# Kernel tuning notes

Hardware: AMD Instinct MI355X
Metric: run time of the kernel (lower is better)

Reference implementation:

```python
import jax, jax.numpy as jnp
import numpy as np

N = 50000      # nodes
E = 800000     # edges (avg degree 16)
DIN = 512      # input_dim
DH = 256       # hidden_dim
KMAX = 50      # max_clusters; K = max(5, min(50, ceil(N/50))) = 50 for N=50000


def _gcn_propagate(h, src, dst, n):
    """Symmetric-normalized GCN aggregation with self-loops (PyG GCNConv).
    h: already linearly transformed node features (n, d)."""
    loop = jnp.arange(n)
    s = jnp.concatenate([src, loop])
    d = jnp.concatenate([dst, loop])
    deg = jax.ops.segment_sum(jnp.ones_like(d, dtype=h.dtype), d, num_segments=n)
    dinv = jnp.where(deg > 0, deg ** -0.5, 0.0)
    norm = dinv[s] * dinv[d]                      # (E+N,)
    return jax.ops.segment_sum(norm[:, None] * h[s], d, num_segments=n)


def setup_inputs() -> dict:
    key = jax.random.key(0)
    ks = jax.random.split(key, 6)
    x = jax.random.normal(ks[0], (N, DIN), dtype=jnp.float32)
    edge_index = jax.random.randint(ks[1], (2, E), 0, N, dtype=jnp.int64)
    positions = jax.random.uniform(ks[2], (N, 2), dtype=jnp.float32)
    # GCNConv params (glorot-ish weights, zero bias as in PyG init)
    W1 = jax.random.normal(ks[3], (DIN, DH), dtype=jnp.float32) * np.float32(1.0 / np.sqrt(DIN))
    b1 = jnp.zeros((DH,), dtype=jnp.float32)
    W2 = jax.random.normal(ks[4], (DH, KMAX), dtype=jnp.float32) * np.float32(1.0 / np.sqrt(DH))
    b2 = jnp.zeros((KMAX,), dtype=jnp.float32)
    spatial_weight = jnp.asarray(1.0, dtype=jnp.float32)
    return {"x": x, "positions": positions, "W1": W1, "b1": b1,
            "W2": W2, "b2": b2, "spatial_weight": spatial_weight,
            "edge_index": edge_index}


def reference(x, positions, W1, b1, W2, b2, spatial_weight, edge_index):
    src, dst = edge_index[0], edge_index[1]
    n = x.shape[0]
    # layer 1: GCNConv(input_dim -> hidden_dim) + ReLU
    h = jax.nn.relu(_gcn_propagate(x @ W1, src, dst, n) + b1)
    # layer 2: GCNConv(hidden_dim -> max_clusters)
    s = _gcn_propagate(h @ W2, src, dst, n) + b2
    # K = max(5, min(50, ceil(N/50))) = 50 here -> s[:, :K] is identity slice
    S = jax.nn.softmax(s[:, :KMAX], axis=1)       # (N, K), Eq. 7
    # spatial loss (Eq. 9): softmax > 0 always, so the >0 guards are no-ops
    d2 = jnp.sum((positions[src] - positions[dst]) ** 2, axis=1)   # (E,) squared dist
    dot = jnp.sum(S[src] * S[dst], axis=1)                          # (E,) sum_k S_ik S_jk
    L_spatial = spatial_weight * jnp.sum(d2 * dot) / src.shape[0]
    return S, L_spatial
```

## Files before the change

### kernel.cpp

```cpp
#include <hip/hip_runtime.h>
#include <math.h>


typedef __attribute__((ext_vector_type(8))) short bf16x8;
typedef __attribute__((ext_vector_type(4))) float f32x4;
typedef __attribute__((ext_vector_type(4))) unsigned int u32x4;
typedef _Float16 f16;
typedef __attribute__((ext_vector_type(2))) _Float16 f16x2;
typedef __attribute__((ext_vector_type(4))) _Float16 f16x4;
typedef __attribute__((ext_vector_type(8))) _Float16 f16x8;

__device__ inline unsigned short f32_to_bf16(float f) {
    unsigned u = __float_as_uint(f);
    unsigned r = u + 0x7FFFu + ((u >> 16) & 1u);
    return (unsigned short)(r >> 16);
}
__device__ inline float bf16_to_f32(unsigned short h) {
    return __uint_as_float((unsigned)h << 16);
}

__device__ inline void glds16(const void* g, void* l) {
    __builtin_amdgcn_global_load_lds(
        (const __attribute__((address_space(1))) unsigned int*)g,
        (__attribute__((address_space(3))) unsigned int*)l, 16, 0, 0);
}

__global__ void detect_i64_kernel(const unsigned* __restrict__ w, int* __restrict__ flag) {
    __shared__ int red[256];
    int cnt = 0;
    for (int i = threadIdx.x; i < 4096; i += 256)
        cnt += (w[2 * i + 1] == 0u) ? 1 : 0;
    red[threadIdx.x] = cnt;
    __syncthreads();
    for (int s = 128; s > 0; s >>= 1) {
        if ((int)threadIdx.x < s) red[threadIdx.x] += red[threadIdx.x + s];
        __syncthreads();
    }
    if (threadIdx.x == 0) *flag = (red[0] > 2048) ? 1 : 0;
}

__global__ void convert_edges_kernel(const void* __restrict__ ei, int* __restrict__ es,
                                     int* __restrict__ ed, int* __restrict__ cnt,
                                     int E, const int* __restrict__ flag) {
    int idx = blockIdx.x * blockDim.x + threadIdx.x;
    if (idx >= 2 * E) return;
    int v;
    if (*flag) v = (int)((const long long*)ei)[idx];
    else       v = ((const int*)ei)[idx];
    if (idx < E) es[idx] = v;
    else { ed[idx - E] = v; atomicAdd(&cnt[v], 1); }
}

__global__ __launch_bounds__(1024) void scan_block_kernel(const int* __restrict__ cnt,
        int* __restrict__ row_ptr, int* __restrict__ btot, int n) {
    __shared__ int buf[1024];
    int i = blockIdx.x * 1024 + threadIdx.x;
    buf[threadIdx.x] = (i < n) ? cnt[i] : 0;
    __syncthreads();
    for (int off = 1; off < 1024; off <<= 1) {
        int t = ((int)threadIdx.x >= off) ? buf[threadIdx.x - off] : 0;
        __syncthreads();
        buf[threadIdx.x] += t;
        __syncthreads();
    }
    if (i < n) row_ptr[i + 1] = buf[threadIdx.x];
    if (threadIdx.x == 1023) btot[blockIdx.x] = buf[1023];
}

__global__ __launch_bounds__(1024) void scan_tops_kernel(int* __restrict__ btot, int nb) {
    __shared__ int buf[1024];
    buf[threadIdx.x] = ((int)threadIdx.x < nb) ? btot[threadIdx.x] : 0;
    __syncthreads();
    for (int off = 1; off < 1024; off <<= 1) {
        int t = ((int)threadIdx.x >= off) ? buf[threadIdx.x - off] : 0;
        __syncthreads();
        buf[threadIdx.x] += t;
        __syncthreads();
    }
    if ((int)threadIdx.x < nb) btot[threadIdx.x] = buf[threadIdx.x];
}

__global__ void scan_finalize_kernel(int* __restrict__ row_ptr, const int* __restrict__ btot,
        const int* __restrict__ cnt, int* __restrict__ cursor, float* __restrict__ dinv, int n) {
    int i = blockIdx.x * blockDim.x + threadIdx.x;
    if (i >= n) return;
    int blk = i >> 10;
    int off = blk ? btot[blk - 1] : 0;
    int incl = row_ptr[i + 1] + off;
    row_ptr[i + 1] = incl;
    cursor[i] = incl - cnt[i];
    dinv[i] = rsqrtf((float)(cnt[i] + 1));
    if (i == 0) row_ptr[0] = 0;
}

__global__ void scatter_kernel(const int* __restrict__ es, const int* __restrict__ ed,
                               const float* __restrict__ dinv, int* __restrict__ cursor,
                               int* __restrict__ csr_src, float* __restrict__ csr_nrm, int E) {
    int e = blockIdx.x * blockDim.x + threadIdx.x;
    if (e < E) {
        int s = es[e];
        int d = ed[e];
        int p = atomicAdd(&cursor[d], 1);
        csr_src[p] = s;
        csr_nrm[p] = dinv[s];
    }
}

__global__ void wsplit_kernel(const float* __restrict__ W,
                              unsigned short* __restrict__ Th,
                              unsigned short* __restrict__ Tl, int K, int N, int nk) {
    int idx = blockIdx.x * 256 + threadIdx.x;
    if (idx >= K * N) return;
    int k = idx / N, n = idx % N;
    float f = W[idx];
    unsigned short h = f32_to_bf16(f);
    unsigned short l = f32_to_bf16(f - bf16_to_f32(h));
    int p = n >> 7, np = n & 127, t = k >> 5, kg = (k & 31) >> 3, ke = k & 7;
    size_t o = ((size_t)((p * nk + t) * 4 + kg) << 10) + np * 8 + ke;
    Th[o] = h;
    Tl[o] = l;
}

__global__ void wsplit2_kernel(const float* __restrict__ W2,
                               f16* __restrict__ W2t_hi, f16* __restrict__ W2t_lo,
                               int K, int NC) {
    int idx = blockIdx.x * 256 + threadIdx.x;
    if (idx >= 64 * K) return;
    int n = idx / K, k = idx % K;
    float v = (n < NC) ? W2[(size_t)k * NC + n] : 0.f;
    f16 h = (f16)v;
    W2t_hi[idx] = h;
    W2t_lo[idx] = (f16)(v - (float)h);
}

#define G1_BM 128
#define G1_BN 128
#define G1_BK 32

__global__ __launch_bounds__(256) void gemm1_mfma(
        const float* __restrict__ X, const unsigned short* __restrict__ WtH,
        const unsigned short* __restrict__ WtL, f16* __restrict__ C,
        int M, int K, int N) {
    __shared__ __align__(16) unsigned char lds[32768];

    const int tid  = threadIdx.x;
    const int lane = tid & 63;
    const int wave = tid >> 6;
    const int wm   = wave & 1;
    const int wn   = wave >> 1;
    const int m0   = blockIdx.x * G1_BM;
    const int pn   = blockIdx.y;
    const int nk   = K / G1_BK;

    const float* Xbase[4];
    #pragma unroll
    for (int i = 0; i < 4; ++i) {
        int c   = i * 256 + tid;
        int row = c >> 3;
        int sl  = (c & 7) ^ (row & 7);
        int gr  = m0 + row;
        if (gr > M - 1) gr = M - 1;
        Xbase[i] = X + (size_t)gr * K + sl * 4;
    }
    const unsigned short* BhBase = WtH + ((size_t)pn * nk << 12) + (size_t)tid * 8;
    const unsigned short* BlBase = WtL + ((size_t)pn * nk << 12) + (size_t)tid * 8;

    f32x4 acc[4][4] = {};
    const int kq   = lane >> 4;
    const int frow = lane & 15;
    const int bOff = 16384 + (kq << 11) + ((wn * 64 + frow) << 4);

    for (int t = 0; t < nk; ++t) {
        const int k0 = t * G1_BK;
        #pragma unroll
        for (int i = 0; i < 4; ++i)
            glds16(Xbase[i] + k0, lds + i * 4096 + wave * 1024);
        const unsigned short* bh = BhBase + (size_t)t * 4096;
        const unsigned short* bl = BlBase + (size_t)t * 4096;
        glds16(bh,        lds + 16384 + wave * 1024);
        glds16(bh + 2048, lds + 20480 + wave * 1024);
        glds16(bl,        lds + 24576 + wave * 1024);
        glds16(bl + 2048, lds + 28672 + wave * 1024);
        __syncthreads();

        bf16x8 bhf[4], blf[4];
        #pragma unroll
        for (int nn = 0; nn < 4; ++nn) {
            bhf[nn] = *(const bf16x8*)(lds + bOff + nn * 256);
            blf[nn] = *(const bf16x8*)(lds + bOff + 8192 + nn * 256);
        }
        #pragma unroll
        for (int mm = 0; mm < 4; ++mm) {
            int ra = wm * 64 + mm * 16 + frow;
            int rb = ra << 7;
            int sw = (ra & 7) << 4;
            int s0 = kq << 1;
            f32x4 p0 = *(const f32x4*)(lds + rb + ((s0 << 4) ^ sw));
            f32x4 p1 = *(const f32x4*)(lds + rb + (((s0 + 1) << 4) ^ sw));
            float f[8] = {p0[0], p0[1], p0[2], p0[3], p1[0], p1[1], p1[2], p1[3]};
            u32x4 hv, lv;
            #pragma unroll
            for (int p = 0; p < 4; ++p) {
                unsigned b0 = __float_as_uint(f[2 * p]);
                unsigned b1 = __float_as_uint(f[2 * p + 1]);
                hv[p] = __builtin_amdgcn_perm(b1, b0, 0x07060302u);
                float l0 = f[2 * p]     - __uint_as_float(b0 & 0xFFFF0000u);
                float l1 = f[2 * p + 1] - __uint_as_float(b1 & 0xFFFF0000u);
                lv[p] = __builtin_amdgcn_perm(__float_as_uint(l1),
                                              __float_as_uint(l0), 0x07060302u);
            }
            union { u32x4 u; bf16x8 b; } ah, al;
            ah.u = hv; al.u = lv;
            #pragma unroll
            for (int nn = 0; nn < 4; ++nn)
                acc[mm][nn] = __builtin_amdgcn_mfma_f32_16x16x32_bf16(ah.b, bhf[nn], acc[mm][nn], 0, 0, 0);
            #pragma unroll
            for (int nn = 0; nn < 4; ++nn)
                acc[mm][nn] = __builtin_amdgcn_mfma_f32_16x16x32_bf16(ah.b, blf[nn], acc[mm][nn], 0, 0, 0);
            #pragma unroll
            for (int nn = 0; nn < 4; ++nn)
                acc[mm][nn] = __builtin_amdgcn_mfma_f32_16x16x32_bf16(al.b, bhf[nn], acc[mm][nn], 0, 0, 0);
        }
        __syncthreads();
    }

    const int n0 = pn * G1_BN;
    #pragma unroll
    for (int mm = 0; mm < 4; ++mm) {
        #pragma unroll
        for (int i = 0; i < 4; ++i) {
            int gr = m0 + wm * 64 + mm * 16 + kq * 4 + i;
            if (gr >= M) continue;
            #pragma unroll
            for (int nn = 0; nn < 4; ++nn) {
                int gc = n0 + wn * 64 + nn * 16 + frow;
                C[(size_t)gr * N + gc] = (f16)acc[mm][nn][i];
            }
        }
    }
}

__global__ __launch_bounds__(256) void gemm2_mfma(
        const f16* __restrict__ h, const f16* __restrict__ W2t_hi,
        const f16* __restrict__ W2t_lo, f16* __restrict__ g,
        int M, int K, int NC) {
    const int tid  = threadIdx.x;
    const int lane = tid & 63;
    const int wave = tid >> 6;
    const int wm   = wave & 1;
    const int wn   = wave >> 1;
    const int m0   = blockIdx.x * 64;

    const int koff = (lane >> 4) * 8;
    const int frow = lane & 15;

    f32x4 acc[2][2] = {};

    const f16* a_base[2];
    #pragma unroll
    for (int mm = 0; mm < 2; ++mm) {
        int gr = m0 + wm * 32 + mm * 16 + frow;
        a_base[mm] = h + (size_t)(gr < M ? gr : 0) * K + koff;
    }
    const f16* bh_base[2];
    const f16* bl_base[2];
    #pragma unroll
    for (int nn = 0; nn < 2; ++nn) {
        int r = wn * 32 + nn * 16 + frow;
        bh_base[nn] = W2t_hi + (size_t)r * K + koff;
        bl_base[nn] = W2t_lo + (size_t)r * K + koff;
    }

    const int nk = K / 32;
    for (int t = 0; t < nk; ++t) {
        const int kk = t * 32;
        f16x8 a[2], bh[2], bl[2];
        #pragma unroll
        for (int mm = 0; mm < 2; ++mm) a[mm] = *(const f16x8*)(a_base[mm] + kk);
        #pragma unroll
        for (int nn = 0; nn < 2; ++nn) {
            bh[nn] = *(const f16x8*)(bh_base[nn] + kk);
            bl[nn] = *(const f16x8*)(bl_base[nn] + kk);
        }
        #pragma unroll
        for (int mm = 0; mm < 2; ++mm)
            #pragma unroll
            for (int nn = 0; nn < 2; ++nn) {
                acc[mm][nn] = __builtin_amdgcn_mfma_f32_16x16x32_f16(a[mm], bh[nn], acc[mm][nn], 0, 0, 0);
                acc[mm][nn] = __builtin_amdgcn_mfma_f32_16x16x32_f16(a[mm], bl[nn], acc[mm][nn], 0, 0, 0);
            }
    }

    #pragma unroll
    for (int mm = 0; mm < 2; ++mm) {
        #pragma unroll
        for (int i = 0; i < 4; ++i) {
            int gr = m0 + wm * 32 + mm * 16 + (lane >> 4) * 4 + i;
            if (gr >= M) continue;
            #pragma unroll
            for (int nn = 0; nn < 2; ++nn) {
                int gc = wn * 32 + nn * 16 + frow;
                if (gc < NC) g[(size_t)gr * NC + gc] = (f16)acc[mm][nn][i];
            }
        }
    }
}

__device__ inline float4 ld_h4(const f16x4* __restrict__ p) {
    f16x4 v = *p;
    return make_float4((float)v.x, (float)v.y, (float)v.z, (float)v.w);
}

__global__ __launch_bounds__(256) void agg1_kernel(const f16* __restrict__ h0,
        const float* __restrict__ dinv, const int* __restrict__ row_ptr,
        const int* __restrict__ csr_src, const float* __restrict__ csr_nrm,
        const float* __restrict__ b1, f16* __restrict__ h, int n) {
    int wid = (int)((blockIdx.x * (size_t)blockDim.x + threadIdx.x) >> 6);
    int lane = threadIdx.x & 63;
    if (wid >= n) return;
    const f16x4* h0v = (const f16x4*)h0;
    float di = dinv[wid];
    float4 v = ld_h4(&h0v[(size_t)wid * 64 + lane]);
    float self = di * di;
    float4 acc;
    acc.x = self * v.x; acc.y = self * v.y; acc.z = self * v.z; acc.w = self * v.w;
    int beg = row_ptr[wid], end = row_ptr[wid + 1];
    int j = beg;
    for (; j + 2 <= end; j += 2) {
        int s0 = csr_src[j], s1 = csr_src[j + 1];
        float n0 = csr_nrm[j] * di, n1 = csr_nrm[j + 1] * di;
        float4 u0 = ld_h4(&h0v[(size_t)s0 * 64 + lane]);
        float4 u1 = ld_h4(&h0v[(size_t)s1 * 64 + lane]);
        acc.x = fmaf(n0, u0.x, acc.x); acc.y = fmaf(n0, u0.y, acc.y);
        acc.z = fmaf(n0, u0.z, acc.z); acc.w = fmaf(n0, u0.w, acc.w);
        acc.x = fmaf(n1, u1.x, acc.x); acc.y = fmaf(n1, u1.y, acc.y);
        acc.z = fmaf(n1, u1.z, acc.z); acc.w = fmaf(n1, u1.w, acc.w);
    }
    if (j < end) {
        int s0 = csr_src[j];
        float n0 = csr_nrm[j] * di;
        float4 u0 = ld_h4(&h0v[(size_t)s0 * 64 + lane]);
        acc.x = fmaf(n0, u0.x, acc.x); acc.y = fmaf(n0, u0.y, acc.y);
        acc.z = fmaf(n0, u0.z, acc.z); acc.w = fmaf(n0, u0.w, acc.w);
    }
    float4 bb = ((const float4*)b1)[lane];
    f16x4 out;
    out.x = (f16)fmaxf(acc.x + bb.x, 0.f);
    out.y = (f16)fmaxf(acc.y + bb.y, 0.f);
    out.z = (f16)fmaxf(acc.z + bb.z, 0.f);
    out.w = (f16)fmaxf(acc.w + bb.w, 0.f);
    ((f16x4*)h)[(size_t)wid * 64 + lane] = out;
}

__global__ __launch_bounds__(256) void agg2_softmax_kernel(const f16* __restrict__ g,
        const float* __restrict__ dinv, const int* __restrict__ row_ptr,
        const int* __restrict__ csr_src, const float* __restrict__ csr_nrm,
        const float* __restrict__ b2, float* __restrict__ S, f16* __restrict__ Sh,
        int n, int KC) {
    int wid = (int)((blockIdx.x * (size_t)blockDim.x + threadIdx.x) >> 6);
    int lane = threadIdx.x & 63;
    if (wid >= n) return;
    bool act = lane < KC;
    size_t gidx = act ? (size_t)lane : 0;
    float di = dinv[wid];
    float a0 = 0.f, a1 = 0.f, a2 = 0.f, a3 = 0.f;
    if (act) a0 = di * di * (float)g[(size_t)wid * KC + lane];
    int beg = row_ptr[wid], end = row_ptr[wid + 1];
    int j = beg;
    for (; j + 4 <= end; j += 4) {
        int s0 = csr_src[j], s1 = csr_src[j + 1], s2 = csr_src[j + 2], s3 = csr_src[j + 3];
        float4 nv = *(const float4*)(csr_nrm + j);
        float n0 = csr_nrm[j]     * di;
        float n1 = csr_nrm[j + 1] * di;
        float n2 = csr_nrm[j + 2] * di;
        float n3 = csr_nrm[j + 3] * di;
        (void)nv;
        float g0 = (float)g[(size_t)s0 * KC + gidx];
        float g1 = (float)g[(size_t)s1 * KC + gidx];
        float g2 = (float)g[(size_t)s2 * KC + gidx];
        float g3 = (float)g[(size_t)s3 * KC + gidx];
        a0 = fmaf(n0, g0, a0);
        a1 = fmaf(n1, g1, a1);
        a2 = fmaf(n2, g2, a2);
        a3 = fmaf(n3, g3, a3);
    }
    for (; j < end; ++j) {
        int s0 = csr_src[j];
        float n0 = csr_nrm[j] * di;
        a0 = fmaf(n0, (float)g[(size_t)s0 * KC + gidx], a0);
    }
    float acc = (a0 + a1) + (a2 + a3);
    float val = act ? (acc + b2[lane]) : -INFINITY;
    float m = val;
    #pragma unroll
    for (int o = 32; o > 0; o >>= 1) m = fmaxf(m, __shfl_xor(m, o));
    float e = act ? expf(val - m) : 0.f;
    float ssum = e;
    #pragma unroll
    for (int o = 32; o > 0; o >>= 1) ssum += __shfl_xor(ssum, o);
    if (act) {
        float sv = e / ssum;
        S[(size_t)wid * KC + lane] = sv;
        Sh[(size_t)wid * KC + lane] = (f16)sv;
    }
}

__global__ __launch_bounds__(256) void loss_partial_kernel(const int* __restrict__ es,
        const int* __restrict__ ed, const float* __restrict__ pos,
        const f16* __restrict__ Sh, float* __restrict__ parts, int E, int KC) {
    float local = 0.f;
    int stride = gridDim.x * blockDim.x;
    for (int e = blockIdx.x * blockDim.x + threadIdx.x; e < E; e += stride) {
        int s = es[e], d = ed[e];
        float2 ps = ((const float2*)pos)[s];
        float2 pd = ((const float2*)pos)[d];
        float dx = ps.x - pd.x, dy = ps.y - pd.y;
        float d2 = dx * dx + dy * dy;
        const f16x2* Sa = (const f16x2*)(Sh + (size_t)s * KC);
        const f16x2* Sb = (const f16x2*)(Sh + (size_t)d * KC);
        float dot = 0.f;
        #pragma unroll
        for (int k = 0; k < 25; ++k) {
            f16x2 a = Sa[k], b = Sb[k];
            dot = fmaf((float)a.x, (float)b.x, dot);
            dot = fmaf((float)a.y, (float)b.y, dot);
        }
        local = fmaf(d2, dot, local);
    }
    __shared__ float red[256];
    red[threadIdx.x] = local;
    __syncthreads();
    for (int s = 128; s > 0; s >>= 1) {
        if ((int)threadIdx.x < s) red[threadIdx.x] += red[threadIdx.x + s];
        __syncthreads();
    }
    if (threadIdx.x == 0) parts[blockIdx.x] = red[0];
}

__global__ __launch_bounds__(1024) void loss_final_kernel(const float* __restrict__ parts,
        const float* __restrict__ sw, float* __restrict__ out, float invE) {
    __shared__ float red[1024];
    red[threadIdx.x] = parts[threadIdx.x];
    __syncthreads();
    for (int s = 512; s > 0; s >>= 1) {
        if ((int)threadIdx.x < s) red[threadIdx.x] += red[threadIdx.x + s];
        __syncthreads();
    }
    if (threadIdx.x == 0) out[0] = sw[0] * red[0] * invE;
}

extern "C" void kernel_launch(void* const* d_in, const int* in_sizes, int n_in,
                              void* d_out, int out_size, void* d_ws, size_t ws_size,
                              hipStream_t stream) {
    const float* x   = (const float*)d_in[0];
    const float* pos = (const float*)d_in[1];
    const float* W1  = (const float*)d_in[2];
    const float* b1  = (const float*)d_in[3];
    const float* W2  = (const float*)d_in[4];
    const float* b2  = (const float*)d_in[5];
    const float* sw  = (const float*)d_in[6];
    const void*  ei  = d_in[7];

    const int DH  = in_sizes[3];
    const int KC  = in_sizes[5];
    const int DIN = in_sizes[2] / DH;
    const int n   = in_sizes[0] / DIN;
    const int E   = in_sizes[7] / 2;

    char* p = (char*)d_ws;
    auto alloc = [&](size_t bytes) {
        char* r = p;
        p += (bytes + 255) & ~(size_t)255;
        return r;
    };
    int*   flag    = (int*)alloc(256);
    int*   es      = (int*)alloc((size_t)E * 4);
    int*   ed      = (int*)alloc((size_t)E * 4);
    int*   cnt     = (int*)alloc((size_t)n * 4);
    int*   cursor  = (int*)alloc((size_t)n * 4);
    int*   row_ptr = (int*)alloc(((size_t)n + 1) * 4);
    int*   btot    = (int*)alloc(1024 * 4);
    int*   csr     = (int*)alloc((size_t)E * 4);
    float* csr_nrm = (float*)alloc((size_t)E * 4);
    float* dinv    = (float*)alloc((size_t)n * 4);
    float* parts   = (float*)alloc(1024 * 4);
    unsigned short* Wt_hi = (unsigned short*)alloc((size_t)DIN * DH * 2);
    unsigned short* Wt_lo = (unsigned short*)alloc((size_t)DIN * DH * 2);
    f16*   W2t_hi  = (f16*)alloc((size_t)64 * DH * 2);
    f16*   W2t_lo  = (f16*)alloc((size_t)64 * DH * 2);
    f16*   h0      = (f16*)alloc((size_t)n * DH * 2);
    f16*   h       = (f16*)alloc((size_t)n * DH * 2);
    f16*   g       = (f16*)alloc((size_t)n * KC * 2);
    f16*   Sh      = (f16*)alloc((size_t)n * KC * 2);

    float* S    = (float*)d_out;
    float* Lout = S + (size_t)n * KC;

    const int nb = (n + 1023) / 1024;
    const int nk = DIN / G1_BK;

    hipMemsetAsync(cnt, 0, (size_t)n * 4, stream);
    detect_i64_kernel<<<1, 256, 0, stream>>>((const unsigned*)ei, flag);
    convert_edges_kernel<<<(2 * E + 255) / 256, 256, 0, stream>>>(ei, es, ed, cnt, E, flag);
    scan_block_kernel<<<nb, 1024, 0, stream>>>(cnt, row_ptr, btot, n);
    scan_tops_kernel<<<1, 1024, 0, stream>>>(btot, nb);
    scan_finalize_kernel<<<(n + 255) / 256, 256, 0, stream>>>(row_ptr, btot, cnt, cursor, dinv, n);
    scatter_kernel<<<(E + 255) / 256, 256, 0, stream>>>(es, ed, dinv, cursor, csr, csr_nrm, E);

    wsplit_kernel<<<(DIN * DH + 255) / 256, 256, 0, stream>>>(W1, Wt_hi, Wt_lo, DIN, DH, nk);
    wsplit2_kernel<<<(64 * DH + 255) / 256, 256, 0, stream>>>(W2, W2t_hi, W2t_lo, DH, KC);

    dim3 g1((n + G1_BM - 1) / G1_BM, DH / G1_BN);
    gemm1_mfma<<<g1, 256, 0, stream>>>(x, Wt_hi, Wt_lo, h0, n, DIN, DH);

    agg1_kernel<<<(int)(((size_t)n * 64 + 255) / 256), 256, 0, stream>>>(
        h0, dinv, row_ptr, csr, csr_nrm, b1, h, n);

    gemm2_mfma<<<(n + 63) / 64, 256, 0, stream>>>(h, W2t_hi, W2t_lo, g, n, DH, KC);

    agg2_softmax_kernel<<<(int)(((size_t)n * 64 + 255) / 256), 256, 0, stream>>>(
        g, dinv, row_ptr, csr, csr_nrm, b2, S, Sh, n, KC);

    loss_partial_kernel<<<1024, 256, 0, stream>>>(es, ed, pos, Sh, parts, E, KC);
    loss_final_kernel<<<1, 1024, 0, stream>>>(parts, sw, Lout, 1.0f / (float)E);
}
```

Before: 348.6 us.

## Fuse layer-1 aggregation into GEMM2 via LDS tile and pad Sh rows to 64

Merges the first GCN aggregation with the second GEMM. Each block aggregates 64 nodes into a shared-memory tile and feeds it straight to the MFMA GEMM, so the intermediate hidden tensor is never written to or read back from global memory. The aggregation loop is also unrolled to four neighbours. Separately, the f16 softmax copy is padded to 64 columns, which lets the loss kernel use 16-byte vector loads. The trade-off is lower occupancy from the LDS tile, plus load imbalance because each wave handles 16 nodes serially before the GEMM starts.

```diff
diff --git a/kernel.cpp b/kernel.cpp
--- a/kernel.cpp
+++ b/kernel.cpp
@@ -240,28 +240,78 @@
     }
 }
 
-__global__ __launch_bounds__(256) void gemm2_mfma(
-        const f16* __restrict__ h, const f16* __restrict__ W2t_hi,
-        const f16* __restrict__ W2t_lo, f16* __restrict__ g,
-        int M, int K, int NC) {
+__device__ inline float4 ld_h4(const f16x4* __restrict__ p) {
+    f16x4 v = *p;
+    return make_float4((float)v.x, (float)v.y, (float)v.z, (float)v.w);
+}
+
+__global__ __launch_bounds__(256) void agg1_gemm2_kernel(
+        const f16* __restrict__ h0, const float* __restrict__ dinv,
+        const int* __restrict__ row_ptr, const int* __restrict__ csr_src,
+        const float* __restrict__ csr_nrm, const float* __restrict__ b1,
+        const f16* __restrict__ W2t_hi, const f16* __restrict__ W2t_lo,
+        f16* __restrict__ g, int n, int K, int KC) {
+    __shared__ __align__(16) f16 hs[64][264];
+
     const int tid  = threadIdx.x;
     const int lane = tid & 63;
     const int wave = tid >> 6;
+    const int base = blockIdx.x * 64;
+
+    const f16x4* h0v = (const f16x4*)h0;
+    float4 bb = ((const float4*)b1)[lane];
+    for (int i = 0; i < 16; ++i) {
+        int wid = base + wave * 16 + i;
+        f16x4 out = {0, 0, 0, 0};
+        if (wid < n) {
+            float di = dinv[wid];
+            float4 v = ld_h4(&h0v[(size_t)wid * 64 + lane]);
+            float self = di * di;
+            float4 acc;
+            acc.x = self * v.x; acc.y = self * v.y; acc.z = self * v.z; acc.w = self * v.w;
+            int beg = row_ptr[wid], end = row_ptr[wid + 1];
+            int j = beg;
+            for (; j + 4 <= end; j += 4) {
+                int s0 = csr_src[j],     s1 = csr_src[j + 1];
+                int s2 = csr_src[j + 2], s3 = csr_src[j + 3];
+                float n0 = csr_nrm[j] * di,     n1 = csr_nrm[j + 1] * di;
+                float n2 = csr_nrm[j + 2] * di, n3 = csr_nrm[j + 3] * di;
+                float4 u0 = ld_h4(&h0v[(size_t)s0 * 64 + lane]);
+                float4 u1 = ld_h4(&h0v[(size_t)s1 * 64 + lane]);
+                float4 u2 = ld_h4(&h0v[(size_t)s2 * 64 + lane]);
+                float4 u3 = ld_h4(&h0v[(size_t)s3 * 64 + lane]);
+                acc.x = fmaf(n0, u0.x, acc.x); acc.y = fmaf(n0, u0.y, acc.y);
+                acc.z = fmaf(n0, u0.z, acc.z); acc.w = fmaf(n0, u0.w, acc.w);
+                acc.x = fmaf(n1, u1.x, acc.x); acc.y = fmaf(n1, u1.y, acc.y);
+                acc.z = fmaf(n1, u1.z, acc.z); acc.w = fmaf(n1, u1.w, acc.w);
+                acc.x = fmaf(n2, u2.x, acc.x); acc.y = fmaf(n2, u2.y, acc.y);
+                acc.z = fmaf(n2, u2.z, acc.z); acc.w = fmaf(n2, u2.w, acc.w);
+                acc.x = fmaf(n3, u3.x, acc.x); acc.y = fmaf(n3, u3.y, acc.y);
+                acc.z = fmaf(n3, u3.z, acc.z); acc.w = fmaf(n3, u3.w, acc.w);
+            }
+            for (; j < end; ++j) {
+                int s0 = csr_src[j];
+                float n0 = csr_nrm[j] * di;
+                float4 u0 = ld_h4(&h0v[(size_t)s0 * 64 + lane]);
+                acc.x = fmaf(n0, u0.x, acc.x); acc.y = fmaf(n0, u0.y, acc.y);
+                acc.z = fmaf(n0, u0.z, acc.z); acc.w = fmaf(n0, u0.w, acc.w);
+            }
+            out.x = (f16)fmaxf(acc.x + bb.x, 0.f);
+            out.y = (f16)fmaxf(acc.y + bb.y, 0.f);
+            out.z = (f16)fmaxf(acc.z + bb.z, 0.f);
+            out.w = (f16)fmaxf(acc.w + bb.w, 0.f);
+        }
+        *(f16x4*)&hs[wave * 16 + i][lane * 4] = out;
+    }
+    __syncthreads();
+
     const int wm   = wave & 1;
     const int wn   = wave >> 1;
-    const int m0   = blockIdx.x * 64;
-
-    const int koff = (lane >> 4) * 8;
+    const int kq   = lane >> 4;
     const int frow = lane & 15;
-
-    f32x4 acc[2][2] = {};
-
-    const f16* a_base[2];
-    #pragma unroll
-    for (int mm = 0; mm < 2; ++mm) {
-        int gr = m0 + wm * 32 + mm * 16 + frow;
-        a_base[mm] = h + (size_t)(gr < M ? gr : 0) * K + koff;
-    }
+    const int koff = kq * 8;
+
+    f32x4 acc2[2][2] = {};
     const f16* bh_base[2];
     const f16* bl_base[2];
     #pragma unroll
@@ -271,12 +321,12 @@
         bl_base[nn] = W2t_lo + (size_t)r * K + koff;
     }
 
-    const int nk = K / 32;
-    for (int t = 0; t < nk; ++t) {
+    for (int t = 0; t < K / 32; ++t) {
         const int kk = t * 32;
         f16x8 a[2], bh[2], bl[2];
         #pragma unroll
-        for (int mm = 0; mm < 2; ++mm) a[mm] = *(const f16x8*)(a_base[mm] + kk);
+        for (int mm = 0; mm < 2; ++mm)
+            a[mm] = *(const f16x8*)&hs[wm * 32 + mm * 16 + frow][kk + koff];
         #pragma unroll
         for (int nn = 0; nn < 2; ++nn) {
             bh[nn] = *(const f16x8*)(bh_base[nn] + kk);
@@ -286,8 +336,8 @@
         for (int mm = 0; mm < 2; ++mm)
             #pragma unroll
             for (int nn = 0; nn < 2; ++nn) {
-                acc[mm][nn] = __builtin_amdgcn_mfma_f32_16x16x32_f16(a[mm], bh[nn], acc[mm][nn], 0, 0, 0);
-                acc[mm][nn] = __builtin_amdgcn_mfma_f32_16x16x32_f16(a[mm], bl[nn], acc[mm][nn], 0, 0, 0);
+                acc2[mm][nn] = __builtin_amdgcn_mfma_f32_16x16x32_f16(a[mm], bh[nn], acc2[mm][nn], 0, 0, 0);
+                acc2[mm][nn] = __builtin_amdgcn_mfma_f32_16x16x32_f16(a[mm], bl[nn], acc2[mm][nn], 0, 0, 0);
             }
     }
 
@@ -295,61 +345,15 @@
     for (int mm = 0; mm < 2; ++mm) {
         #pragma unroll
         for (int i = 0; i < 4; ++i) {
-            int gr = m0 + wm * 32 + mm * 16 + (lane >> 4) * 4 + i;
-            if (gr >= M) continue;
+            int gr = base + wm * 32 + mm * 16 + kq * 4 + i;
+            if (gr >= n) continue;
             #pragma unroll
             for (int nn = 0; nn < 2; ++nn) {
                 int gc = wn * 32 + nn * 16 + frow;
-                if (gc < NC) g[(size_t)gr * NC + gc] = (f16)acc[mm][nn][i];
+                if (gc < KC) g[(size_t)gr * KC + gc] = (f16)acc2[mm][nn][i];
             }
         }
     }
-}
-
-__device__ inline float4 ld_h4(const f16x4* __restrict__ p) {
-    f16x4 v = *p;
-    return make_float4((float)v.x, (float)v.y, (float)v.z, (float)v.w);
-}
-
-__global__ __launch_bounds__(256) void agg1_kernel(const f16* __restrict__ h0,
-        const float* __restrict__ dinv, const int* __restrict__ row_ptr,
-        const int* __restrict__ csr_src, const float* __restrict__ csr_nrm,
-        const float* __restrict__ b1, f16* __restrict__ h, int n) {
-    int wid = (int)((blockIdx.x * (size_t)blockDim.x + threadIdx.x) >> 6);
-    int lane = threadIdx.x & 63;
-    if (wid >= n) return;
-    const f16x4* h0v = (const f16x4*)h0;
-    float di = dinv[wid];
-    float4 v = ld_h4(&h0v[(size_t)wid * 64 + lane]);
-    float self = di * di;
-    float4 acc;
-    acc.x = self * v.x; acc.y = self * v.y; acc.z = self * v.z; acc.w = self * v.w;
-    int beg = row_ptr[wid], end = row_ptr[wid + 1];
-    int j = beg;
-    for (; j + 2 <= end; j += 2) {
-        int s0 = csr_src[j], s1 = csr_src[j + 1];
-        float n0 = csr_nrm[j] * di, n1 = csr_nrm[j + 1] * di;
-        float4 u0 = ld_h4(&h0v[(size_t)s0 * 64 + lane]);
-        float4 u1 = ld_h4(&h0v[(size_t)s1 * 64 + lane]);
-        acc.x = fmaf(n0, u0.x, acc.x); acc.y = fmaf(n0, u0.y, acc.y);
-        acc.z = fmaf(n0, u0.z, acc.z); acc.w = fmaf(n0, u0.w, acc.w);
-        acc.x = fmaf(n1, u1.x, acc.x); acc.y = fmaf(n1, u1.y, acc.y);
-        acc.z = fmaf(n1, u1.z, acc.z); acc.w = fmaf(n1, u1.w, acc.w);
-    }
-    if (j < end) {
-        int s0 = csr_src[j];
-        float n0 = csr_nrm[j] * di;
-        float4 u0 = ld_h4(&h0v[(size_t)s0 * 64 + lane]);
-        acc.x = fmaf(n0, u0.x, acc.x); acc.y = fmaf(n0, u0.y, acc.y);
-        acc.z = fmaf(n0, u0.z, acc.z); acc.w = fmaf(n0, u0.w, acc.w);
-    }
-    float4 bb = ((const float4*)b1)[lane];
-    f16x4 out;
-    out.x = (f16)fmaxf(acc.x + bb.x, 0.f);
-    out.y = (f16)fmaxf(acc.y + bb.y, 0.f);
-    out.z = (f16)fmaxf(acc.z + bb.z, 0.f);
-    out.w = (f16)fmaxf(acc.w + bb.w, 0.f);
-    ((f16x4*)h)[(size_t)wid * 64 + lane] = out;
 }
 
 __global__ __launch_bounds__(256) void agg2_softmax_kernel(const f16* __restrict__ g,
@@ -369,12 +373,10 @@
     int j = beg;
     for (; j + 4 <= end; j += 4) {
         int s0 = csr_src[j], s1 = csr_src[j + 1], s2 = csr_src[j + 2], s3 = csr_src[j + 3];
-        float4 nv = *(const float4*)(csr_nrm + j);
         float n0 = csr_nrm[j]     * di;
         float n1 = csr_nrm[j + 1] * di;
         float n2 = csr_nrm[j + 2] * di;
         float n3 = csr_nrm[j + 3] * di;
-        (void)nv;
         float g0 = (float)g[(size_t)s0 * KC + gidx];
         float g1 = (float)g[(size_t)s1 * KC + gidx];
         float g2 = (float)g[(size_t)s2 * KC + gidx];
@@ -398,16 +400,16 @@
     float ssum = e;
     #pragma unroll
     for (int o = 32; o > 0; o >>= 1) ssum += __shfl_xor(ssum, o);
-    if (act) {
-        float sv = e / ssum;
-        S[(size_t)wid * KC + lane] = sv;
-        Sh[(size_t)wid * KC + lane] = (f16)sv;
+    if (lane < 64) {
+        float sv = act ? (e / ssum) : 0.f;
+        if (act) S[(size_t)wid * KC + lane] = sv;
+        Sh[(size_t)wid * 64 + lane] = (f16)sv;
     }
 }
 
 __global__ __launch_bounds__(256) void loss_partial_kernel(const int* __restrict__ es,
         const int* __restrict__ ed, const float* __restrict__ pos,
-        const f16* __restrict__ Sh, float* __restrict__ parts, int E, int KC) {
+        const f16* __restrict__ Sh, float* __restrict__ parts, int E) {
     float local = 0.f;
     int stride = gridDim.x * blockDim.x;
     for (int e = blockIdx.x * blockDim.x + threadIdx.x; e < E; e += stride) {
@@ -416,14 +418,15 @@
         float2 pd = ((const float2*)pos)[d];
         float dx = ps.x - pd.x, dy = ps.y - pd.y;
         float d2 = dx * dx + dy * dy;
-        const f16x2* Sa = (const f16x2*)(Sh + (size_t)s * KC);
-        const f16x2* Sb = (const f16x2*)(Sh + (size_t)d * KC);
+        const f16x8* Sa = (const f16x8*)(Sh + (size_t)s * 64);
+        const f16x8* Sb = (const f16x8*)(Sh + (size_t)d * 64);
         float dot = 0.f;
         #pragma unroll
-        for (int k = 0; k < 25; ++k) {
-            f16x2 a = Sa[k], b = Sb[k];
-            dot = fmaf((float)a.x, (float)b.x, dot);
-            dot = fmaf((float)a.y, (float)b.y, dot);
+        for (int q = 0; q < 7; ++q) {
+            f16x8 a = Sa[q], b = Sb[q];
+            #pragma unroll
+            for (int k = 0; k < 8; ++k)
+                dot = fmaf((float)a[k], (float)b[k], dot);
         }
         local = fmaf(d2, dot, local);
     }
@@ -489,9 +492,8 @@
     f16*   W2t_hi  = (f16*)alloc((size_t)64 * DH * 2);
     f16*   W2t_lo  = (f16*)alloc((size_t)64 * DH * 2);
     f16*   h0      = (f16*)alloc((size_t)n * DH * 2);
-    f16*   h       = (f16*)alloc((size_t)n * DH * 2);
     f16*   g       = (f16*)alloc((size_t)n * KC * 2);
-    f16*   Sh      = (f16*)alloc((size_t)n * KC * 2);
+    f16*   Sh      = (f16*)alloc((size_t)n * 64 * 2);
 
     float* S    = (float*)d_out;
     float* Lout = S + (size_t)n * KC;
@@ -513,14 +515,12 @@
     dim3 g1((n + G1_BM - 1) / G1_BM, DH / G1_BN);
     gemm1_mfma<<<g1, 256, 0, stream>>>(x, Wt_hi, Wt_lo, h0, n, DIN, DH);
 
-    agg1_kernel<<<(int)(((size_t)n * 64 + 255) / 256), 256, 0, stream>>>(
-        h0, dinv, row_ptr, csr, csr_nrm, b1, h, n);
-
-    gemm2_mfma<<<(n + 63) / 64, 256, 0, stream>>>(h, W2t_hi, W2t_lo, g, n, DH, KC);
+    agg1_gemm2_kernel<<<(n + 63) / 64, 256, 0, stream>>>(
+        h0, dinv, row_ptr, csr, csr_nrm, b1, W2t_hi, W2t_lo, g, n, DH, KC);
 
     agg2_softmax_kernel<<<(int)(((size_t)n * 64 + 255) / 256), 256, 0, stream>>>(
         g, dinv, row_ptr, csr, csr_nrm, b2, S, Sh, n, KC);
 
-    loss_partial_kernel<<<1024, 256, 0, stream>>>(es, ed, pos, Sh, parts, E, KC);
+    loss_partial_kernel<<<1024, 256, 0, stream>>>(es, ed, pos, Sh, parts, E);
     loss_final_kernel<<<1, 1024, 0, stream>>>(parts, sw, Lout, 1.0f / (float)E);
 }
```

Result: faster. 336.5 us (-3.5%).
